# Performance work log

Measured on AMD Instinct MI355X. Metric: run time of the kernel, lower is better.

## Reference

```python
import jax, jax.numpy as jnp
import numpy as np

N = 20000
E = 320000
NEG_SLOPE = 0.2
LN_EPS = 1e-5


def gat_conv(x, W, a_src, a_dst, b, src, dst, heads, ch, concat):
    # x: [N, F_in]; W: [F_in, H*C]; a_src/a_dst: [H, C]; b: [H*C] or [C]
    xl = (x @ W).reshape(N, heads, ch)                      # [N,H,C]
    alpha_src = jnp.sum(xl * a_src, axis=-1)                # [N,H]
    alpha_dst = jnp.sum(xl * a_dst, axis=-1)                # [N,H]
    e = alpha_src[src] + alpha_dst[dst]                     # [E',H]
    e = jax.nn.leaky_relu(e, NEG_SLOPE)
    # segment softmax over incoming edges of each dst node
    m = jax.ops.segment_max(e, dst, num_segments=N)         # [N,H]
    m = jnp.where(jnp.isfinite(m), m, 0.0)
    ex = jnp.exp(e - m[dst])
    denom = jax.ops.segment_sum(ex, dst, num_segments=N)    # [N,H]
    alpha = ex / (denom[dst] + 1e-16)                       # [E',H]
    msg = alpha[:, :, None] * xl[src]                       # [E',H,C]
    out = jax.ops.segment_sum(msg, dst, num_segments=N)     # [N,H,C]
    if concat:
        return out.reshape(N, heads * ch) + b
    return out.mean(axis=1) + b


def layer_norm(x, g, b):
    mu = jnp.mean(x, axis=-1, keepdims=True)
    var = jnp.mean(jnp.square(x - mu), axis=-1, keepdims=True)
    return (x - mu) * jax.lax.rsqrt(var + LN_EPS) * g + b


def setup_inputs() -> dict:
    key = jax.random.key(0)
    ks = jax.random.split(key, 24)
    d = {}
    d["x"] = jax.random.normal(ks[0], (N, 50), dtype=jnp.float32)
    d["edge_index"] = jax.random.randint(ks[1], (2, E), 0, N, dtype=jnp.int64)

    def glorot(k, shape):
        fan = shape[0] + shape[-1]
        return jax.random.normal(k, shape, dtype=jnp.float32) * np.sqrt(2.0 / fan)

    # conv1: 50 -> 256, heads=4, concat
    d["W1"] = glorot(ks[2], (50, 4 * 256))
    d["a_src1"] = glorot(ks[3], (4, 256))
    d["a_dst1"] = glorot(ks[4], (4, 256))
    d["b1"] = jnp.zeros((4 * 256,), jnp.float32)
    # conv2: 1024 -> 256, heads=4, concat
    d["W2"] = glorot(ks[5], (1024, 4 * 256))
    d["a_src2"] = glorot(ks[6], (4, 256))
    d["a_dst2"] = glorot(ks[7], (4, 256))
    d["b2"] = jnp.zeros((4 * 256,), jnp.float32)
    # conv3: 1024 -> 121, heads=6, concat=False
    d["W3"] = glorot(ks[8], (1024, 6 * 121))
    d["a_src3"] = glorot(ks[9], (6, 121))
    d["a_dst3"] = glorot(ks[10], (6, 121))
    d["b3"] = jnp.zeros((121,), jnp.float32)
    # skips
    d["skipW1"] = glorot(ks[11], (50, 1024))
    d["skipb1"] = jnp.zeros((1024,), jnp.float32)
    d["skipW2"] = glorot(ks[12], (1024, 1024))
    d["skipb2"] = jnp.zeros((1024,), jnp.float32)
    # layer norms
    d["g1"] = jnp.ones((1024,), jnp.float32)
    d["beta1"] = jnp.zeros((1024,), jnp.float32)
    d["g2"] = jnp.ones((1024,), jnp.float32)
    d["beta2"] = jnp.zeros((1024,), jnp.float32)
    return d


def reference(x, edge_index, W1, a_src1, a_dst1, b1, W2, a_src2, a_dst2, b2,
              W3, a_src3, a_dst3, b3, skipW1, skipb1, skipW2, skipb2,
              g1, beta1, g2, beta2):
    # add self loops (PyG GATConv default)
    loop = jnp.arange(N, dtype=edge_index.dtype)
    src = jnp.concatenate([edge_index[0], loop])
    dst = jnp.concatenate([edge_index[1], loop])

    h = gat_conv(x, W1, a_src1, a_dst1, b1, src, dst, 4, 256, True)
    h = jax.nn.elu(layer_norm(h + (x @ skipW1 + skipb1), g1, beta1))
    h2 = gat_conv(h, W2, a_src2, a_dst2, b2, src, dst, 4, 256, True)
    h2 = jax.nn.elu(layer_norm(h2 + (h @ skipW2 + skipb2), g2, beta2))
    out = gat_conv(h2, W3, a_src3, a_dst3, b3, src, dst, 6, 121, False)
    return out
```

## Files before the change

### kernel.cpp

```cpp
#include <hip/hip_runtime.h>
#include <hip/hip_bf16.h>
#include <math.h>

typedef __attribute__((ext_vector_type(8))) __bf16 bf16x8;
typedef __attribute__((ext_vector_type(4))) float f32x4;
typedef __attribute__((ext_vector_type(4))) int i32x4;

#if __has_builtin(__builtin_amdgcn_global_load_lds)
#define HAVE_GLD 1
#define GLD16(g, l)                                                                      \
    __builtin_amdgcn_global_load_lds(                                                    \
        (const __attribute__((address_space(1))) unsigned int*)(g),                      \
        (__attribute__((address_space(3))) unsigned int*)(l), 16, 0, 0)
#else
#define HAVE_GLD 0
#endif

__global__ __launch_bounds__(256) void gemm_bt(const __bf16* __restrict__ A,
                                               const __bf16* __restrict__ Bt,
                                               __bf16* __restrict__ C,
                                               int M, int N, int K) {
    __shared__ __bf16 As[128 * 32];
    __shared__ __bf16 Bs[128 * 32];
    const int t = threadIdx.x;
    const int lane = t & 63;
    const int wid = t >> 6;
    const int wm = (wid >> 1) << 6;
    const int wn = (wid & 1) << 6;
    const int bm = blockIdx.x * 128;
    const int bn = blockIdx.y * 128;

    const int srow = (wid << 4) + (lane >> 2);
    const int scol = (lane & 3) << 3;

    f32x4 acc[4][4];
#pragma unroll
    for (int i = 0; i < 4; i++)
#pragma unroll
        for (int j = 0; j < 4; j++) acc[i][j] = (f32x4){0.f, 0.f, 0.f, 0.f};

    const int m16 = lane & 15;
    const int k8 = (lane >> 4) << 3;

    for (int k0 = 0; k0 < K; k0 += 32) {
        __syncthreads();
#if HAVE_GLD
        GLD16(A + (size_t)(bm + srow) * K + k0 + scol, As + srow * 32 + scol);
        GLD16(A + (size_t)(bm + 64 + srow) * K + k0 + scol, As + (64 + srow) * 32 + scol);
        GLD16(Bt + (size_t)(bn + srow) * K + k0 + scol, Bs + srow * 32 + scol);
        GLD16(Bt + (size_t)(bn + 64 + srow) * K + k0 + scol, Bs + (64 + srow) * 32 + scol);
#else
        {
            bf16x8 a0 = *(const bf16x8*)(A + (size_t)(bm + srow) * K + k0 + scol);
            bf16x8 a1 = *(const bf16x8*)(A + (size_t)(bm + 64 + srow) * K + k0 + scol);
            bf16x8 b0 = *(const bf16x8*)(Bt + (size_t)(bn + srow) * K + k0 + scol);
            bf16x8 b1 = *(const bf16x8*)(Bt + (size_t)(bn + 64 + srow) * K + k0 + scol);
            *(bf16x8*)(As + srow * 32 + scol) = a0;
            *(bf16x8*)(As + (64 + srow) * 32 + scol) = a1;
            *(bf16x8*)(Bs + srow * 32 + scol) = b0;
            *(bf16x8*)(Bs + (64 + srow) * 32 + scol) = b1;
        }
#endif
        __syncthreads();
        bf16x8 af[4], bfr[4];
#pragma unroll
        for (int i = 0; i < 4; i++) {
            af[i] = *(const bf16x8*)(As + (wm + 16 * i + m16) * 32 + k8);
            bfr[i] = *(const bf16x8*)(Bs + (wn + 16 * i + m16) * 32 + k8);
        }
#pragma unroll
        for (int i = 0; i < 4; i++)
#pragma unroll
            for (int j = 0; j < 4; j++)
                acc[i][j] = __builtin_amdgcn_mfma_f32_16x16x32_bf16(af[i], bfr[j], acc[i][j], 0, 0, 0);
    }
    const int r4 = (lane >> 4) << 2;
#pragma unroll
    for (int i = 0; i < 4; i++) {
#pragma unroll
        for (int j = 0; j < 4; j++) {
            int col = bn + wn + 16 * j + m16;
#pragma unroll
            for (int r = 0; r < 4; r++) {
                int row = bm + wm + 16 * i + r4 + r;
                C[(size_t)row * N + col] = (__bf16)acc[i][j][r];
            }
        }
    }
}

__global__ void pack_x_k(const float* __restrict__ x, __bf16* __restrict__ xp, int rows_real) {
    int i = blockIdx.x * 256 + threadIdx.x;
    int n = i >> 6, c = i & 63;
    float v = 0.f;
    if (n < rows_real && c < 50) v = x[n * 50 + c];
    xp[(size_t)n * 64 + c] = (__bf16)v;
}

__global__ void transpose_pad_k(const float* __restrict__ W, __bf16* __restrict__ WT,
                                int K, int N, int Kp, int Np) {
    __shared__ float tile[32][33];
    int bx = blockIdx.x, by = blockIdx.y;
    int tx = threadIdx.x & 31, ty = threadIdx.x >> 5;
#pragma unroll
    for (int r = ty; r < 32; r += 8) {
        int k = by * 32 + r, n = bx * 32 + tx;
        float v = 0.f;
        if (k < K && n < N) v = W[(size_t)k * N + n];
        tile[r][tx] = v;
    }
    __syncthreads();
#pragma unroll
    for (int r = ty; r < 32; r += 8) {
        int n = bx * 32 + r, k = by * 32 + tx;
        if (n < Np && k < Kp) WT[(size_t)n * Kp + k] = (__bf16)tile[tx][r];
    }
}

__global__ void transpose_pad_w3_k(const float* __restrict__ W, __bf16* __restrict__ WT) {
    __shared__ float tile[32][33];
    int bx = blockIdx.x, by = blockIdx.y;
    int tx = threadIdx.x & 31, ty = threadIdx.x >> 5;
    int r0 = bx * 32;
    int h = r0 >> 7;
    int c0 = r0 & 127;
#pragma unroll
    for (int r = ty; r < 32; r += 8) {
        int k = by * 32 + r;
        int c = c0 + tx;
        float v = 0.f;
        if (c < 121) v = W[(size_t)k * 726 + h * 121 + c];
        tile[r][tx] = v;
    }
    __syncthreads();
#pragma unroll
    for (int r = ty; r < 32; r += 8) {
        int rr = r0 + r;
        int k = by * 32 + tx;
        WT[(size_t)rr * 1024 + k] = (__bf16)tile[tx][r];
    }
}

__global__ void probe_ei_k(const int* __restrict__ ei, int* __restrict__ flag) {
    if (blockIdx.x == 0 && threadIdx.x == 0) {
        int all0 = 1;
        for (int i = 0; i < 64; i++)
            if (ei[2 * i + 1] != 0) { all0 = 0; break; }
        *flag = all0;
    }
}

__device__ __forceinline__ int load_ei(const int* ei, int idx, int is64) {
    return is64 ? ei[2 * idx] : ei[idx];
}

__global__ void hist_k(const int* __restrict__ ei, const int* __restrict__ flag,
                       int* __restrict__ cnt, int E, int Nn) {
    int e = blockIdx.x * 256 + threadIdx.x;
    if (e >= E + Nn) return;
    int is64 = *flag;
    int d = (e < E) ? load_ei(ei, E + e, is64) : (e - E);
    d = min(max(d, 0), Nn - 1);
    atomicAdd(&cnt[d], 1);
}

__global__ __launch_bounds__(1024) void scan_k(const int* __restrict__ cnt, int* __restrict__ row_ptr,
                                               int Nn) {
    __shared__ int part[1024];
    int t = threadIdx.x;
    int chunk = (Nn + 1023) >> 10;
    int lo = t * chunk;
    int hi = lo + chunk; if (hi > Nn) hi = Nn; if (lo > Nn) lo = Nn;
    int s = 0;
    for (int i = lo; i < hi; i++) s += (cnt[i] + 15) & ~15;
    part[t] = s;
    __syncthreads();
    for (int off = 1; off < 1024; off <<= 1) {
        int v = (t >= off) ? part[t - off] : 0;
        __syncthreads();
        part[t] += v;
        __syncthreads();
    }
    int run = part[t] - s;
    for (int i = lo; i < hi; i++) { row_ptr[i] = run; run += (cnt[i] + 15) & ~15; }
    if (t == 1023) row_ptr[Nn] = part[1023];
}

__global__ void fill_csr_k(const int* __restrict__ ei, const int* __restrict__ flag,
                           const int* __restrict__ row_ptr, int* __restrict__ cursor,
                           int* __restrict__ src_csr, int E, int Nn) {
    int e = blockIdx.x * 256 + threadIdx.x;
    if (e >= E + Nn) return;
    int is64 = *flag;
    int d = (e < E) ? load_ei(ei, E + e, is64) : (e - E);
    int s = (e < E) ? load_ei(ei, e, is64) : (e - E);
    d = min(max(d, 0), Nn - 1);
    s = min(max(s, 0), Nn - 1);
    int slot = row_ptr[d] + atomicAdd(&cursor[d], 1);
    src_csr[slot] = s;
}

__global__ void alpha_k(const __bf16* __restrict__ XL, int ld, const float* __restrict__ a_src,
                        const float* __restrict__ a_dst, float* __restrict__ asrc,
                        float* __restrict__ adst, int Nn, int H, int C, int Cpad) {
    int gw = (blockIdx.x * 256 + threadIdx.x) >> 6;
    int lane = threadIdx.x & 63;
    if (gw >= Nn * H) return;
    int n = gw / H, h = gw - n * H;
    const __bf16* row = XL + (size_t)n * ld + h * Cpad;
    const float* as = a_src + h * C;
    const float* ad = a_dst + h * C;
    float s = 0.f, d = 0.f;
    for (int c = lane; c < C; c += 64) {
        float v = (float)row[c];
        s += v * as[c];
        d += v * ad[c];
    }
#pragma unroll
    for (int off = 32; off; off >>= 1) {
        s += __shfl_down(s, off);
        d += __shfl_down(d, off);
    }
    if (lane == 0) { asrc[n * H + h] = s; adst[n * H + h] = d; }
}

__global__ void attn_k(const int* __restrict__ row_ptr, const int* __restrict__ deg,
                       const int* __restrict__ src_csr,
                       const float* __restrict__ asrc, const float* __restrict__ adst,
                       float* __restrict__ wt, int Nn, int H, int Epad) {
    int gw = (blockIdx.x * 256 + threadIdx.x) >> 6;
    int lane = threadIdx.x & 63;
    if (gw >= Nn) return;
    int n = gw;
    int base = row_ptr[n], dg = deg[n];
    for (int h = 0; h < H; h++) {
        float ad = adst[n * H + h];
        float m = -1e30f;
        for (int s = lane; s < dg; s += 64) {
            float e = asrc[src_csr[base + s] * H + h] + ad;
            e = e > 0.f ? e : 0.2f * e;
            m = fmaxf(m, e);
        }
#pragma unroll
        for (int off = 1; off < 64; off <<= 1) m = fmaxf(m, __shfl_xor(m, off));
        float sum = 0.f;
        for (int s = lane; s < dg; s += 64) {
            float e = asrc[src_csr[base + s] * H + h] + ad;
            e = e > 0.f ? e : 0.2f * e;
            sum += __expf(e - m);
        }
#pragma unroll
        for (int off = 1; off < 64; off <<= 1) sum += __shfl_xor(sum, off);
        float inv = 1.f / (sum + 1e-16f);
        float* wrow = wt + (size_t)h * Epad;
        for (int s = lane; s < dg; s += 64) {
            float e = asrc[src_csr[base + s] * H + h] + ad;
            e = e > 0.f ? e : 0.2f * e;
            wrow[base + s] = __expf(e - m) * inv;
        }
    }
}

__global__ __launch_bounds__(256) void agg_skip6(const __bf16* __restrict__ XL,
                                                 const float* __restrict__ wt,
                                                 const int* __restrict__ row_ptr,
                                                 const int* __restrict__ src_csr,
                                                 const float* __restrict__ bias,
                                                 const float* __restrict__ sb,
                                                 __bf16* __restrict__ SK, int Nn, int Epad) {
    const int cc = blockIdx.x;
    const int n = blockIdx.y * 4 + (threadIdx.x >> 6);
    const int lane = threadIdx.x & 63;
    if (n >= Nn) return;
    const int g = lane >> 4;
    const int p = lane & 15;
    const int col = cc * 128 + p * 8;
    const float* wrow = wt + (size_t)(cc >> 1) * Epad;
    const __bf16* XLc = XL + col;
    const int base = row_ptr[n], end = row_ptr[n + 1];

    float acc[8];
#pragma unroll
    for (int j = 0; j < 8; j++) acc[j] = 0.f;

    for (int e = base; e < end; e += 16) {
        i32x4 si = *(const i32x4*)(src_csr + e + 4 * g);
        f32x4 wv = *(const f32x4*)(wrow + e + 4 * g);
#pragma unroll
        for (int s = 0; s < 4; s++) {
            bf16x8 xv = *(const bf16x8*)(XLc + (size_t)si[s] * 1024);
#pragma unroll
            for (int j = 0; j < 8; j++) acc[j] += wv[s] * (float)xv[j];
        }
    }
#pragma unroll
    for (int j = 0; j < 8; j++) {
        acc[j] += __shfl_xor(acc[j], 16);
        acc[j] += __shfl_xor(acc[j], 32);
    }
    if (lane < 16) {
        size_t o = (size_t)n * 1024 + col;
        bf16x8 sk = *(const bf16x8*)(SK + o);
        bf16x8 res;
#pragma unroll
        for (int j = 0; j < 8; j++)
            res[j] = (__bf16)(acc[j] + bias[col + j] + sb[col + j] + (float)sk[j]);
        *(bf16x8*)(SK + o) = res;
    }
}

__global__ __launch_bounds__(256) void agg_mean6(const __bf16* __restrict__ XL,
                                                 const float* __restrict__ wt,
                                                 const int* __restrict__ row_ptr,
                                                 const int* __restrict__ src_csr,
                                                 __bf16* __restrict__ part, int Nn, int Epad) {
    const int cc = blockIdx.x;
    const int n = blockIdx.y * 4 + (threadIdx.x >> 6);
    const int lane = threadIdx.x & 63;
    if (n >= Nn) return;
    const int g = lane >> 4;
    const int p = lane & 15;
    const int col = cc * 128 + p * 8;
    const float* wrow = wt + (size_t)cc * Epad;
    const __bf16* XLc = XL + col;
    const int base = row_ptr[n], end = row_ptr[n + 1];

    float acc[8];
#pragma unroll
    for (int j = 0; j < 8; j++) acc[j] = 0.f;

    for (int e = base; e < end; e += 16) {
        i32x4 si = *(const i32x4*)(src_csr + e + 4 * g);
        f32x4 wv = *(const f32x4*)(wrow + e + 4 * g);
#pragma unroll
        for (int s = 0; s < 4; s++) {
            bf16x8 xv = *(const bf16x8*)(XLc + (size_t)si[s] * 768);
#pragma unroll
            for (int j = 0; j < 8; j++) acc[j] += wv[s] * (float)xv[j];
        }
    }
#pragma unroll
    for (int j = 0; j < 8; j++) {
        acc[j] += __shfl_xor(acc[j], 16);
        acc[j] += __shfl_xor(acc[j], 32);
    }
    if (lane < 16) {
        size_t o = (size_t)n * 768 + col;
        bf16x8 res;
#pragma unroll
        for (int j = 0; j < 8; j++) res[j] = (__bf16)acc[j];
        *(bf16x8*)(part + o) = res;
    }
}

__global__ __launch_bounds__(128) void reduce_mean_k(const __bf16* __restrict__ part,
                                                     const float* __restrict__ b3,
                                                     float* __restrict__ out, int Nn) {
    int n = blockIdx.x;
    int t = threadIdx.x;
    if (t >= 121) return;
    const __bf16* row = part + (size_t)n * 768;
    float s = 0.f;
#pragma unroll
    for (int h = 0; h < 6; h++) s += (float)row[h * 128 + t];
    out[(size_t)n * 121 + t] = s * (1.f / 6.f) + b3[t];
}

__global__ __launch_bounds__(256) void ln_elu_k(const __bf16* __restrict__ in,
                                                const float* __restrict__ g,
                                                const float* __restrict__ be,
                                                __bf16* __restrict__ out, int rows_real) {
    const int D = 1024;
    int n = blockIdx.x;
    int t = threadIdx.x;
    size_t ro = (size_t)n * D;
    if (n >= rows_real) {
#pragma unroll
        for (int j = 0; j < 4; j++) out[ro + t + 256 * j] = (__bf16)0.f;
        return;
    }
    float v[4];
    float s = 0.f, q = 0.f;
#pragma unroll
    for (int j = 0; j < 4; j++) {
        int c = t + 256 * j;
        float a = (float)in[ro + c];
        v[j] = a;
        s += a;
        q += a * a;
    }
#pragma unroll
    for (int off = 32; off; off >>= 1) {
        s += __shfl_down(s, off);
        q += __shfl_down(q, off);
    }
    __shared__ float rs[8];
    int wid = t >> 6;
    if ((t & 63) == 0) { rs[wid] = s; rs[wid + 4] = q; }
    __syncthreads();
    s = rs[0] + rs[1] + rs[2] + rs[3];
    q = rs[4] + rs[5] + rs[6] + rs[7];
    float mu = s * (1.f / 1024.f);
    float var = q * (1.f / 1024.f) - mu * mu;
    float inv = rsqrtf(fmaxf(var, 0.f) + 1e-5f);
#pragma unroll
    for (int j = 0; j < 4; j++) {
        int c = t + 256 * j;
        float y = (v[j] - mu) * inv * g[c] + be[c];
        y = y > 0.f ? y : expm1f(y);
        out[ro + c] = (__bf16)y;
    }
}

extern "C" void kernel_launch(void* const* d_in, const int* in_sizes, int n_in,
                              void* d_out, int out_size, void* d_ws, size_t ws_size,
                              hipStream_t stream) {
    const float* x   = (const float*)d_in[0];
    const int*   ei  = (const int*)d_in[1];
    const float* W1  = (const float*)d_in[2];
    const float* as1 = (const float*)d_in[3];
    const float* ad1 = (const float*)d_in[4];
    const float* b1  = (const float*)d_in[5];
    const float* W2  = (const float*)d_in[6];
    const float* as2 = (const float*)d_in[7];
    const float* ad2 = (const float*)d_in[8];
    const float* b2  = (const float*)d_in[9];
    const float* W3  = (const float*)d_in[10];
    const float* as3 = (const float*)d_in[11];
    const float* ad3 = (const float*)d_in[12];
    const float* b3  = (const float*)d_in[13];
    const float* sW1 = (const float*)d_in[14];
    const float* sb1 = (const float*)d_in[15];
    const float* sW2 = (const float*)d_in[16];
    const float* sb2 = (const float*)d_in[17];
    const float* g1  = (const float*)d_in[18];
    const float* be1 = (const float*)d_in[19];
    const float* g2  = (const float*)d_in[20];
    const float* be2 = (const float*)d_in[21];
    float* out = (float*)d_out;

    const int Nn = 20000;
    const int E = in_sizes[1] / 2;
    const int E2 = E + Nn;
    const int Ecap = E2 + 16 * Nn;
    const int Mpad = 20096;

    char* p = (char*)d_ws;
    auto alloc = [&](size_t bytes) {
        char* r = p;
        p += (bytes + 255) & ~(size_t)255;
        return r;
    };
    __bf16* W1pT  = (__bf16*)alloc((size_t)1024 * 64 * 2);
    __bf16* sW1T  = (__bf16*)alloc((size_t)1024 * 64 * 2);
    __bf16* W2T   = (__bf16*)alloc((size_t)1024 * 1024 * 2);
    __bf16* sW2T  = (__bf16*)alloc((size_t)1024 * 1024 * 2);
    __bf16* W3pT  = (__bf16*)alloc((size_t)768 * 1024 * 2);
    __bf16* xp    = (__bf16*)alloc((size_t)Mpad * 64 * 2);
    __bf16* XL    = (__bf16*)alloc((size_t)Mpad * 1024 * 2);
    __bf16* SK    = (__bf16*)alloc((size_t)Mpad * 1024 * 2);
    __bf16* H1    = (__bf16*)alloc((size_t)Mpad * 1024 * 2);
    float*  asrcb = (float*)alloc((size_t)Nn * 6 * 4);
    float*  adstb = (float*)alloc((size_t)Nn * 6 * 4);
    float*  wbuf  = (float*)alloc((size_t)6 * Ecap * 4);
    int*    rowp  = (int*)alloc((size_t)(Nn + 1) * 4);
    int*    cnt   = (int*)alloc((size_t)Nn * 4);
    int*    scsr  = (int*)alloc((size_t)Ecap * 4);
    int*    eiflag= (int*)alloc(256);
    __bf16* part  = SK;
    (void)ws_size; (void)n_in; (void)out_size;

    pack_x_k<<<(Mpad * 64) / 256, 256, 0, stream>>>(x, xp, Nn);
    transpose_pad_k<<<dim3(32, 2), 256, 0, stream>>>(W1, W1pT, 50, 1024, 64, 1024);
    transpose_pad_k<<<dim3(32, 2), 256, 0, stream>>>(sW1, sW1T, 50, 1024, 64, 1024);
    transpose_pad_k<<<dim3(32, 32), 256, 0, stream>>>(W2, W2T, 1024, 1024, 1024, 1024);
    transpose_pad_k<<<dim3(32, 32), 256, 0, stream>>>(sW2, sW2T, 1024, 1024, 1024, 1024);
    transpose_pad_w3_k<<<dim3(24, 32), 256, 0, stream>>>(W3, W3pT);

    probe_ei_k<<<1, 64, 0, stream>>>(ei, eiflag);
    hipMemsetAsync(cnt, 0, (size_t)Nn * 4, stream);
    hist_k<<<(E2 + 255) / 256, 256, 0, stream>>>(ei, eiflag, cnt, E, Nn);
    scan_k<<<1, 1024, 0, stream>>>(cnt, rowp, Nn);
    hipMemsetAsync(cnt, 0, (size_t)Nn * 4, stream);
    hipMemsetAsync(scsr, 0, (size_t)Ecap * 4, stream);
    hipMemsetAsync(wbuf, 0, (size_t)6 * Ecap * 4, stream);
    fill_csr_k<<<(E2 + 255) / 256, 256, 0, stream>>>(ei, eiflag, rowp, cnt, scsr, E, Nn);

    gemm_bt<<<dim3(Mpad / 128, 8), 256, 0, stream>>>(xp, W1pT, XL, Mpad, 1024, 64);
    gemm_bt<<<dim3(Mpad / 128, 8), 256, 0, stream>>>(xp, sW1T, SK, Mpad, 1024, 64);
    alpha_k<<<(Nn * 4 * 64) / 256, 256, 0, stream>>>(XL, 1024, as1, ad1, asrcb, adstb, Nn, 4, 256, 256);
    attn_k<<<(Nn + 3) / 4, 256, 0, stream>>>(rowp, cnt, scsr, asrcb, adstb, wbuf, Nn, 4, Ecap);
    agg_skip6<<<dim3(8, (Nn + 3) / 4), 256, 0, stream>>>(XL, wbuf, rowp, scsr, b1, sb1, SK, Nn, Ecap);
    ln_elu_k<<<Mpad, 256, 0, stream>>>(SK, g1, be1, H1, Nn);

    gemm_bt<<<dim3(Mpad / 128, 8), 256, 0, stream>>>(H1, W2T, XL, Mpad, 1024, 1024);
    gemm_bt<<<dim3(Mpad / 128, 8), 256, 0, stream>>>(H1, sW2T, SK, Mpad, 1024, 1024);
    alpha_k<<<(Nn * 4 * 64) / 256, 256, 0, stream>>>(XL, 1024, as2, ad2, asrcb, adstb, Nn, 4, 256, 256);
    attn_k<<<(Nn + 3) / 4, 256, 0, stream>>>(rowp, cnt, scsr, asrcb, adstb, wbuf, Nn, 4, Ecap);
    agg_skip6<<<dim3(8, (Nn + 3) / 4), 256, 0, stream>>>(XL, wbuf, rowp, scsr, b2, sb2, SK, Nn, Ecap);
    ln_elu_k<<<Mpad, 256, 0, stream>>>(SK, g2, be2, H1, Nn);

    gemm_bt<<<dim3(Mpad / 128, 6), 256, 0, stream>>>(H1, W3pT, XL, Mpad, 768, 1024);
    alpha_k<<<(Nn * 6 * 64) / 256, 256, 0, stream>>>(XL, 768, as3, ad3, asrcb, adstb, Nn, 6, 121, 128);
    attn_k<<<(Nn + 3) / 4, 256, 0, stream>>>(rowp, cnt, scsr, asrcb, adstb, wbuf, Nn, 6, Ecap);
    agg_mean6<<<dim3(6, (Nn + 3) / 4), 256, 0, stream>>>(XL, wbuf, rowp, scsr, part, Nn, Ecap);
    reduce_mean_k<<<Nn, 128, 0, stream>>>(part, b3, out, Nn);
}
```

Baseline: 839.5 us.

## Merge prep kernels, fuse paired GEMMs, shrink CSR padding to 8, add fast attention path

Folds the x packing and all weight transposes into one prep kernel. Each pair of GAT and skip GEMMs now runs as a single launch over a concatenated weight matrix. The counter memset is folded into the probe and scan kernels. CSR row padding drops from 16 to 8, so the aggregation loops process 2 neighbours per group instead of 4, which cuts wasted padded gathers. Attention gets a single-pass register path for nodes with degree up to 64, avoiding reloads of the neighbour scores.

```diff
diff --git a/kernel.cpp b/kernel.cpp
--- a/kernel.cpp
+++ b/kernel.cpp
@@ -4,122 +4,110 @@
 
 typedef __attribute__((ext_vector_type(8))) __bf16 bf16x8;
 typedef __attribute__((ext_vector_type(4))) float f32x4;
-typedef __attribute__((ext_vector_type(4))) int i32x4;
 
 #if __has_builtin(__builtin_amdgcn_global_load_lds)
-#define HAVE_GLD 1
 #define GLD16(g, l)                                                                      \
     __builtin_amdgcn_global_load_lds(                                                    \
         (const __attribute__((address_space(1))) unsigned int*)(g),                      \
         (__attribute__((address_space(3))) unsigned int*)(l), 16, 0, 0)
 #else
-#define HAVE_GLD 0
+#define GLD16(g, l) (*(bf16x8*)(l) = *(const bf16x8*)(g))
 #endif
+
+#define GEMM_BODY(A, Bt, K, STORE)                                                       \
+    __shared__ __bf16 As[128 * 32];                                                      \
+    __shared__ __bf16 Bs[128 * 32];                                                      \
+    const int t = threadIdx.x;                                                           \
+    const int lane = t & 63;                                                             \
+    const int wid = t >> 6;                                                              \
+    const int wm = (wid >> 1) << 6;                                                      \
+    const int wn = (wid & 1) << 6;                                                       \
+    const int bm = blockIdx.x * 128;                                                     \
+    const int bn = blockIdx.y * 128;                                                     \
+    const int srow = (wid << 4) + (lane >> 2);                                           \
+    const int scol = (lane & 3) << 3;                                                    \
+    f32x4 acc[4][4];                                                                     \
+    _Pragma("unroll") for (int i = 0; i < 4; i++)                                        \
+        _Pragma("unroll") for (int j = 0; j < 4; j++)                                    \
+            acc[i][j] = (f32x4){0.f, 0.f, 0.f, 0.f};                                     \
+    const int m16 = lane & 15;                                                           \
+    const int k8 = (lane >> 4) << 3;                                                     \
+    for (int k0 = 0; k0 < K; k0 += 32) {                                                 \
+        __syncthreads();                                                                 \
+        GLD16(A + (size_t)(bm + srow) * K + k0 + scol, As + srow * 32 + scol);           \
+        GLD16(A + (size_t)(bm + 64 + srow) * K + k0 + scol, As + (64 + srow) * 32 + scol);\
+        GLD16(Bt + (size_t)(bn + srow) * K + k0 + scol, Bs + srow * 32 + scol);          \
+        GLD16(Bt + (size_t)(bn + 64 + srow) * K + k0 + scol, Bs + (64 + srow) * 32 + scol);\
+        __syncthreads();                                                                 \
+        bf16x8 af[4], bfr[4];                                                            \
+        _Pragma("unroll") for (int i = 0; i < 4; i++) {                                  \
+            af[i] = *(const bf16x8*)(As + (wm + 16 * i + m16) * 32 + k8);                \
+            bfr[i] = *(const bf16x8*)(Bs + (wn + 16 * i + m16) * 32 + k8);               \
+        }                                                                                \
+        _Pragma("unroll") for (int i = 0; i < 4; i++)                                    \
+            _Pragma("unroll") for (int j = 0; j < 4; j++)                                \
+                acc[i][j] = __builtin_amdgcn_mfma_f32_16x16x32_bf16(af[i], bfr[j],       \
+                                                                    acc[i][j], 0, 0, 0); \
+    }                                                                                    \
+    const int r4 = (lane >> 4) << 2;                                                     \
+    STORE
 
 __global__ __launch_bounds__(256) void gemm_bt(const __bf16* __restrict__ A,
                                                const __bf16* __restrict__ Bt,
                                                __bf16* __restrict__ C,
                                                int M, int N, int K) {
-    __shared__ __bf16 As[128 * 32];
-    __shared__ __bf16 Bs[128 * 32];
-    const int t = threadIdx.x;
-    const int lane = t & 63;
-    const int wid = t >> 6;
-    const int wm = (wid >> 1) << 6;
-    const int wn = (wid & 1) << 6;
-    const int bm = blockIdx.x * 128;
-    const int bn = blockIdx.y * 128;
-
-    const int srow = (wid << 4) + (lane >> 2);
-    const int scol = (lane & 3) << 3;
-
-    f32x4 acc[4][4];
-#pragma unroll
-    for (int i = 0; i < 4; i++)
-#pragma unroll
-        for (int j = 0; j < 4; j++) acc[i][j] = (f32x4){0.f, 0.f, 0.f, 0.f};
-
-    const int m16 = lane & 15;
-    const int k8 = (lane >> 4) << 3;
-
-    for (int k0 = 0; k0 < K; k0 += 32) {
-        __syncthreads();
-#if HAVE_GLD
-        GLD16(A + (size_t)(bm + srow) * K + k0 + scol, As + srow * 32 + scol);
-        GLD16(A + (size_t)(bm + 64 + srow) * K + k0 + scol, As + (64 + srow) * 32 + scol);
-        GLD16(Bt + (size_t)(bn + srow) * K + k0 + scol, Bs + srow * 32 + scol);
-        GLD16(Bt + (size_t)(bn + 64 + srow) * K + k0 + scol, Bs + (64 + srow) * 32 + scol);
-#else
-        {
-            bf16x8 a0 = *(const bf16x8*)(A + (size_t)(bm + srow) * K + k0 + scol);
-            bf16x8 a1 = *(const bf16x8*)(A + (size_t)(bm + 64 + srow) * K + k0 + scol);
-            bf16x8 b0 = *(const bf16x8*)(Bt + (size_t)(bn + srow) * K + k0 + scol);
-            bf16x8 b1 = *(const bf16x8*)(Bt + (size_t)(bn + 64 + srow) * K + k0 + scol);
-            *(bf16x8*)(As + srow * 32 + scol) = a0;
-            *(bf16x8*)(As + (64 + srow) * 32 + scol) = a1;
-            *(bf16x8*)(Bs + srow * 32 + scol) = b0;
-            *(bf16x8*)(Bs + (64 + srow) * 32 + scol) = b1;
-        }
-#endif
-        __syncthreads();
-        bf16x8 af[4], bfr[4];
-#pragma unroll
-        for (int i = 0; i < 4; i++) {
-            af[i] = *(const bf16x8*)(As + (wm + 16 * i + m16) * 32 + k8);
-            bfr[i] = *(const bf16x8*)(Bs + (wn + 16 * i + m16) * 32 + k8);
-        }
-#pragma unroll
-        for (int i = 0; i < 4; i++)
-#pragma unroll
-            for (int j = 0; j < 4; j++)
-                acc[i][j] = __builtin_amdgcn_mfma_f32_16x16x32_bf16(af[i], bfr[j], acc[i][j], 0, 0, 0);
-    }
-    const int r4 = (lane >> 4) << 2;
-#pragma unroll
-    for (int i = 0; i < 4; i++) {
-#pragma unroll
-        for (int j = 0; j < 4; j++) {
-            int col = bn + wn + 16 * j + m16;
-#pragma unroll
-            for (int r = 0; r < 4; r++) {
-                int row = bm + wm + 16 * i + r4 + r;
-                C[(size_t)row * N + col] = (__bf16)acc[i][j][r];
-            }
-        }
-    }
-}
-
-__global__ void pack_x_k(const float* __restrict__ x, __bf16* __restrict__ xp, int rows_real) {
-    int i = blockIdx.x * 256 + threadIdx.x;
-    int n = i >> 6, c = i & 63;
-    float v = 0.f;
-    if (n < rows_real && c < 50) v = x[n * 50 + c];
-    xp[(size_t)n * 64 + c] = (__bf16)v;
-}
-
-__global__ void transpose_pad_k(const float* __restrict__ W, __bf16* __restrict__ WT,
-                                int K, int N, int Kp, int Np) {
-    __shared__ float tile[32][33];
-    int bx = blockIdx.x, by = blockIdx.y;
+    GEMM_BODY(A, Bt, K,
+        _Pragma("unroll") for (int i = 0; i < 4; i++)
+            _Pragma("unroll") for (int j = 0; j < 4; j++) {
+                int col = bn + wn + 16 * j + m16;
+                _Pragma("unroll") for (int r = 0; r < 4; r++) {
+                    int row = bm + wm + 16 * i + r4 + r;
+                    C[(size_t)row * N + col] = (__bf16)acc[i][j][r];
+                }
+            })
+}
+
+__global__ __launch_bounds__(256) void gemm_bt2(const __bf16* __restrict__ A,
+                                                const __bf16* __restrict__ Bt,
+                                                __bf16* __restrict__ C0,
+                                                __bf16* __restrict__ C1,
+                                                int M, int K) {
+    GEMM_BODY(A, Bt, K,
+        __bf16* Cp = (bn < 1024) ? C0 : C1;
+        const int cb = bn & 1023;
+        _Pragma("unroll") for (int i = 0; i < 4; i++)
+            _Pragma("unroll") for (int j = 0; j < 4; j++) {
+                int col = cb + wn + 16 * j + m16;
+                _Pragma("unroll") for (int r = 0; r < 4; r++) {
+                    int row = bm + wm + 16 * i + r4 + r;
+                    Cp[(size_t)row * 1024 + col] = (__bf16)acc[i][j][r];
+                }
+            })
+}
+
+__device__ __forceinline__ void transpose_tile(const float* __restrict__ W,
+                                               __bf16* __restrict__ WT,
+                                               int K, int N, int Kp, int Np,
+                                               int bx, int by, float* sm) {
     int tx = threadIdx.x & 31, ty = threadIdx.x >> 5;
 #pragma unroll
     for (int r = ty; r < 32; r += 8) {
         int k = by * 32 + r, n = bx * 32 + tx;
         float v = 0.f;
         if (k < K && n < N) v = W[(size_t)k * N + n];
-        tile[r][tx] = v;
+        sm[r * 33 + tx] = v;
     }
     __syncthreads();
 #pragma unroll
     for (int r = ty; r < 32; r += 8) {
         int n = bx * 32 + r, k = by * 32 + tx;
-        if (n < Np && k < Kp) WT[(size_t)n * Kp + k] = (__bf16)tile[tx][r];
-    }
-}
-
-__global__ void transpose_pad_w3_k(const float* __restrict__ W, __bf16* __restrict__ WT) {
-    __shared__ float tile[32][33];
-    int bx = blockIdx.x, by = blockIdx.y;
+        if (n < Np && k < Kp) WT[(size_t)n * Kp + k] = (__bf16)sm[tx * 33 + r];
+    }
+}
+
+__device__ __forceinline__ void transpose_w3_tile(const float* __restrict__ W,
+                                                  __bf16* __restrict__ WT,
+                                                  int bx, int by, float* sm) {
     int tx = threadIdx.x & 31, ty = threadIdx.x >> 5;
     int r0 = bx * 32;
     int h = r0 >> 7;
@@ -130,22 +118,56 @@
         int c = c0 + tx;
         float v = 0.f;
         if (c < 121) v = W[(size_t)k * 726 + h * 121 + c];
-        tile[r][tx] = v;
+        sm[r * 33 + tx] = v;
     }
     __syncthreads();
 #pragma unroll
     for (int r = ty; r < 32; r += 8) {
         int rr = r0 + r;
         int k = by * 32 + tx;
-        WT[(size_t)rr * 1024 + k] = (__bf16)tile[tx][r];
-    }
-}
-
-__global__ void probe_ei_k(const int* __restrict__ ei, int* __restrict__ flag) {
+        WT[(size_t)rr * 1024 + k] = (__bf16)sm[tx * 33 + r];
+    }
+}
+
+__global__ __launch_bounds__(256) void prep_k(const float* __restrict__ x,
+                                              const float* __restrict__ W1,
+                                              const float* __restrict__ sW1,
+                                              const float* __restrict__ W2,
+                                              const float* __restrict__ sW2,
+                                              const float* __restrict__ W3,
+                                              __bf16* __restrict__ xp,
+                                              __bf16* __restrict__ WTcat1,
+                                              __bf16* __restrict__ WTcat2,
+                                              __bf16* __restrict__ W3pT, int Nn) {
+    __shared__ float sm[32 * 33];
+    int b = blockIdx.x;
+    if (b < 5024) {
+        int i = b * 256 + threadIdx.x;
+        int n = i >> 6, c = i & 63;
+        float v = 0.f;
+        if (n < Nn && c < 50) v = x[n * 50 + c];
+        xp[(size_t)n * 64 + c] = (__bf16)v;
+    } else if (b < 5088) {
+        int i = b - 5024; transpose_tile(W1, WTcat1, 50, 1024, 64, 1024, i % 32, i / 32, sm);
+    } else if (b < 5152) {
+        int i = b - 5088; transpose_tile(sW1, WTcat1 + 1024 * 64, 50, 1024, 64, 1024, i % 32, i / 32, sm);
+    } else if (b < 6176) {
+        int i = b - 5152; transpose_tile(W2, WTcat2, 1024, 1024, 1024, 1024, i % 32, i / 32, sm);
+    } else if (b < 7200) {
+        int i = b - 6176; transpose_tile(sW2, WTcat2 + (size_t)1024 * 1024, 1024, 1024, 1024, 1024, i % 32, i / 32, sm);
+    } else {
+        int i = b - 7200; transpose_w3_tile(W3, W3pT, i % 24, i / 24, sm);
+    }
+}
+
+__global__ void zero_probe_k(const int* __restrict__ ei, int* __restrict__ cnt,
+                             int* __restrict__ flag, int Nn) {
+    int i = blockIdx.x * 256 + threadIdx.x;
+    if (i < Nn) cnt[i] = 0;
     if (blockIdx.x == 0 && threadIdx.x == 0) {
         int all0 = 1;
-        for (int i = 0; i < 64; i++)
-            if (ei[2 * i + 1] != 0) { all0 = 0; break; }
+        for (int k = 0; k < 64; k++)
+            if (ei[2 * k + 1] != 0) { all0 = 0; break; }
         *flag = all0;
     }
 }
@@ -164,7 +186,7 @@
     atomicAdd(&cnt[d], 1);
 }
 
-__global__ __launch_bounds__(1024) void scan_k(const int* __restrict__ cnt, int* __restrict__ row_ptr,
+__global__ __launch_bounds__(1024) void scan_k(int* __restrict__ cnt, int* __restrict__ row_ptr,
                                                int Nn) {
     __shared__ int part[1024];
     int t = threadIdx.x;
@@ -172,7 +194,7 @@
     int lo = t * chunk;
     int hi = lo + chunk; if (hi > Nn) hi = Nn; if (lo > Nn) lo = Nn;
     int s = 0;
-    for (int i = lo; i < hi; i++) s += (cnt[i] + 15) & ~15;
+    for (int i = lo; i < hi; i++) s += (cnt[i] + 7) & ~7;
     part[t] = s;
     __syncthreads();
     for (int off = 1; off < 1024; off <<= 1) {
@@ -182,8 +204,10 @@
         __syncthreads();
     }
     int run = part[t] - s;
-    for (int i = lo; i < hi; i++) { row_ptr[i] = run; run += (cnt[i] + 15) & ~15; }
+    for (int i = lo; i < hi; i++) { row_ptr[i] = run; run += (cnt[i] + 7) & ~7; }
     if (t == 1023) row_ptr[Nn] = part[1023];
+    __syncthreads();
+    for (int i = lo; i < hi; i++) cnt[i] = 0;
 }
 
 __global__ void fill_csr_k(const int* __restrict__ ei, const int* __restrict__ flag,
@@ -227,12 +251,33 @@
 __global__ void attn_k(const int* __restrict__ row_ptr, const int* __restrict__ deg,
                        const int* __restrict__ src_csr,
                        const float* __restrict__ asrc, const float* __restrict__ adst,
-                       float* __restrict__ wt, int Nn, int H, int Epad) {
+                       float* __restrict__ wt, int Nn, int H, int Ecap) {
     int gw = (blockIdx.x * 256 + threadIdx.x) >> 6;
     int lane = threadIdx.x & 63;
     if (gw >= Nn) return;
     int n = gw;
     int base = row_ptr[n], dg = deg[n];
+    if (dg <= 64) {
+        bool v = lane < dg;
+        int src = v ? src_csr[base + lane] : 0;
+        for (int h = 0; h < H; h++) {
+            float ad = adst[n * H + h];
+            float e = -1e30f;
+            if (v) {
+                e = asrc[src * H + h] + ad;
+                e = e > 0.f ? e : 0.2f * e;
+            }
+            float m = e;
+#pragma unroll
+            for (int off = 1; off < 64; off <<= 1) m = fmaxf(m, __shfl_xor(m, off));
+            float ex = v ? __expf(e - m) : 0.f;
+            float sum = ex;
+#pragma unroll
+            for (int off = 1; off < 64; off <<= 1) sum += __shfl_xor(sum, off);
+            if (v) wt[(size_t)h * Ecap + base + lane] = ex / (sum + 1e-16f);
+        }
+        return;
+    }
     for (int h = 0; h < H; h++) {
         float ad = adst[n * H + h];
         float m = -1e30f;
@@ -252,7 +297,7 @@
 #pragma unroll
         for (int off = 1; off < 64; off <<= 1) sum += __shfl_xor(sum, off);
         float inv = 1.f / (sum + 1e-16f);
-        float* wrow = wt + (size_t)h * Epad;
+        float* wrow = wt + (size_t)h * Ecap;
         for (int s = lane; s < dg; s += 64) {
             float e = asrc[src_csr[base + s] * H + h] + ad;
             e = e > 0.f ? e : 0.2f * e;
@@ -261,13 +306,13 @@
     }
 }
 
-__global__ __launch_bounds__(256) void agg_skip6(const __bf16* __restrict__ XL,
+__global__ __launch_bounds__(256) void agg_skip8(const __bf16* __restrict__ XL,
                                                  const float* __restrict__ wt,
                                                  const int* __restrict__ row_ptr,
                                                  const int* __restrict__ src_csr,
                                                  const float* __restrict__ bias,
                                                  const float* __restrict__ sb,
-                                                 __bf16* __restrict__ SK, int Nn, int Epad) {
+                                                 __bf16* __restrict__ SK, int Nn, int Ecap) {
     const int cc = blockIdx.x;
     const int n = blockIdx.y * 4 + (threadIdx.x >> 6);
     const int lane = threadIdx.x & 63;
@@ -275,7 +320,7 @@
     const int g = lane >> 4;
     const int p = lane & 15;
     const int col = cc * 128 + p * 8;
-    const float* wrow = wt + (size_t)(cc >> 1) * Epad;
+    const float* wrow = wt + (size_t)(cc >> 1) * Ecap;
     const __bf16* XLc = XL + col;
     const int base = row_ptr[n], end = row_ptr[n + 1];
 
@@ -283,15 +328,13 @@
 #pragma unroll
     for (int j = 0; j < 8; j++) acc[j] = 0.f;
 
-    for (int e = base; e < end; e += 16) {
-        i32x4 si = *(const i32x4*)(src_csr + e + 4 * g);
-        f32x4 wv = *(const f32x4*)(wrow + e + 4 * g);
-#pragma unroll
-        for (int s = 0; s < 4; s++) {
-            bf16x8 xv = *(const bf16x8*)(XLc + (size_t)si[s] * 1024);
-#pragma unroll
-            for (int j = 0; j < 8; j++) acc[j] += wv[s] * (float)xv[j];
-        }
+    for (int e = base; e < end; e += 8) {
+        int2 si = *(const int2*)(src_csr + e + 2 * g);
+        float2 wv = *(const float2*)(wrow + e + 2 * g);
+        bf16x8 xa = *(const bf16x8*)(XLc + (size_t)si.x * 1024);
+        bf16x8 xb = *(const bf16x8*)(XLc + (size_t)si.y * 1024);
+#pragma unroll
+        for (int j = 0; j < 8; j++) acc[j] += wv.x * (float)xa[j] + wv.y * (float)xb[j];
     }
 #pragma unroll
     for (int j = 0; j < 8; j++) {
@@ -309,11 +352,11 @@
     }
 }
 
-__global__ __launch_bounds__(256) void agg_mean6(const __bf16* __restrict__ XL,
+__global__ __launch_bounds__(256) void agg_mean8(const __bf16* __restrict__ XL,
                                                  const float* __restrict__ wt,
                                                  const int* __restrict__ row_ptr,
                                                  const int* __restrict__ src_csr,
-                                                 __bf16* __restrict__ part, int Nn, int Epad) {
+                                                 __bf16* __restrict__ part, int Nn, int Ecap) {
     const int cc = blockIdx.x;
     const int n = blockIdx.y * 4 + (threadIdx.x >> 6);
     const int lane = threadIdx.x & 63;
@@ -321,7 +364,7 @@
     const int g = lane >> 4;
     const int p = lane & 15;
     const int col = cc * 128 + p * 8;
-    const float* wrow = wt + (size_t)cc * Epad;
+    const float* wrow = wt + (size_t)cc * Ecap;
     const __bf16* XLc = XL + col;
     const int base = row_ptr[n], end = row_ptr[n + 1];
 
@@ -329,15 +372,13 @@
 #pragma unroll
     for (int j = 0; j < 8; j++) acc[j] = 0.f;
 
-    for (int e = base; e < end; e += 16) {
-        i32x4 si = *(const i32x4*)(src_csr + e + 4 * g);
-        f32x4 wv = *(const f32x4*)(wrow + e + 4 * g);
-#pragma unroll
-        for (int s = 0; s < 4; s++) {
-            bf16x8 xv = *(const bf16x8*)(XLc + (size_t)si[s] * 768);
-#pragma unroll
-            for (int j = 0; j < 8; j++) acc[j] += wv[s] * (float)xv[j];
-        }
+    for (int e = base; e < end; e += 8) {
+        int2 si = *(const int2*)(src_csr + e + 2 * g);
+        float2 wv = *(const float2*)(wrow + e + 2 * g);
+        bf16x8 xa = *(const bf16x8*)(XLc + (size_t)si.x * 768);
+        bf16x8 xb = *(const bf16x8*)(XLc + (size_t)si.y * 768);
+#pragma unroll
+        for (int j = 0; j < 8; j++) acc[j] += wv.x * (float)xa[j] + wv.y * (float)xb[j];
     }
 #pragma unroll
     for (int j = 0; j < 8; j++) {
@@ -442,7 +483,7 @@
     const int Nn = 20000;
     const int E = in_sizes[1] / 2;
     const int E2 = E + Nn;
-    const int Ecap = E2 + 16 * Nn;
+    const int Ecap = E2 + 8 * Nn;
     const int Mpad = 20096;
 
     char* p = (char*)d_ws;
@@ -451,58 +492,47 @@
         p += (bytes + 255) & ~(size_t)255;
         return r;
     };
-    __bf16* W1pT  = (__bf16*)alloc((size_t)1024 * 64 * 2);
-    __bf16* sW1T  = (__bf16*)alloc((size_t)1024 * 64 * 2);
-    __bf16* W2T   = (__bf16*)alloc((size_t)1024 * 1024 * 2);
-    __bf16* sW2T  = (__bf16*)alloc((size_t)1024 * 1024 * 2);
-    __bf16* W3pT  = (__bf16*)alloc((size_t)768 * 1024 * 2);
-    __bf16* xp    = (__bf16*)alloc((size_t)Mpad * 64 * 2);
-    __bf16* XL    = (__bf16*)alloc((size_t)Mpad * 1024 * 2);
-    __bf16* SK    = (__bf16*)alloc((size_t)Mpad * 1024 * 2);
-    __bf16* H1    = (__bf16*)alloc((size_t)Mpad * 1024 * 2);
-    float*  asrcb = (float*)alloc((size_t)Nn * 6 * 4);
-    float*  adstb = (float*)alloc((size_t)Nn * 6 * 4);
-    float*  wbuf  = (float*)alloc((size_t)6 * Ecap * 4);
-    int*    rowp  = (int*)alloc((size_t)(Nn + 1) * 4);
-    int*    cnt   = (int*)alloc((size_t)Nn * 4);
-    int*    scsr  = (int*)alloc((size_t)Ecap * 4);
-    int*    eiflag= (int*)alloc(256);
-    __bf16* part  = SK;
+    __bf16* WTcat1 = (__bf16*)alloc((size_t)2048 * 64 * 2);
+    __bf16* WTcat2 = (__bf16*)alloc((size_t)2048 * 1024 * 2);
+    __bf16* W3pT   = (__bf16*)alloc((size_t)768 * 1024 * 2);
+    __bf16* xp     = (__bf16*)alloc((size_t)Mpad * 64 * 2);
+    __bf16* XL     = (__bf16*)alloc((size_t)Mpad * 1024 * 2);
+    __bf16* SK     = (__bf16*)alloc((size_t)Mpad * 1024 * 2);
+    __bf16* H1     = (__bf16*)alloc((size_t)Mpad * 1024 * 2);
+    float*  asrcb  = (float*)alloc((size_t)Nn * 6 * 4);
+    float*  adstb  = (float*)alloc((size_t)Nn * 6 * 4);
+    float*  wbuf   = (float*)alloc((size_t)6 * Ecap * 4);
+    int*    rowp   = (int*)alloc((size_t)(Nn + 1) * 4);
+    int*    cnt    = (int*)alloc((size_t)Nn * 4);
+    int*    scsr   = (int*)alloc((size_t)Ecap * 4);
+    int*    eiflag = (int*)alloc(256);
+    __bf16* part   = SK;
     (void)ws_size; (void)n_in; (void)out_size;
 
-    pack_x_k<<<(Mpad * 64) / 256, 256, 0, stream>>>(x, xp, Nn);
-    transpose_pad_k<<<dim3(32, 2), 256, 0, stream>>>(W1, W1pT, 50, 1024, 64, 1024);
-    transpose_pad_k<<<dim3(32, 2), 256, 0, stream>>>(sW1, sW1T, 50, 1024, 64, 1024);
-    transpose_pad_k<<<dim3(32, 32), 256, 0, stream>>>(W2, W2T, 1024, 1024, 1024, 1024);
-    transpose_pad_k<<<dim3(32, 32), 256, 0, stream>>>(sW2, sW2T, 1024, 1024, 1024, 1024);
-    transpose_pad_w3_k<<<dim3(24, 32), 256, 0, stream>>>(W3, W3pT);
-
-    probe_ei_k<<<1, 64, 0, stream>>>(ei, eiflag);
-    hipMemsetAsync(cnt, 0, (size_t)Nn * 4, stream);
+    prep_k<<<7968, 256, 0, stream>>>(x, W1, sW1, W2, sW2, W3, xp, WTcat1, WTcat2, W3pT, Nn);
+
+    zero_probe_k<<<(Nn + 255) / 256, 256, 0, stream>>>(ei, cnt, eiflag, Nn);
     hist_k<<<(E2 + 255) / 256, 256, 0, stream>>>(ei, eiflag, cnt, E, Nn);
     scan_k<<<1, 1024, 0, stream>>>(cnt, rowp, Nn);
-    hipMemsetAsync(cnt, 0, (size_t)Nn * 4, stream);
-    hipMemsetAsync(scsr, 0, (size_t)Ecap * 4, stream);
-    hipMemsetAsync(wbuf, 0, (size_t)6 * Ecap * 4, stream);
+    (void)hipMemsetAsync(scsr, 0, (size_t)Ecap * 4, stream);
+    (void)hipMemsetAsync(wbuf, 0, (size_t)6 * Ecap * 4, stream);
     fill_csr_k<<<(E2 + 255) / 256, 256, 0, stream>>>(ei, eiflag, rowp, cnt, scsr, E, Nn);
 
-    gemm_bt<<<dim3(Mpad / 128, 8), 256, 0, stream>>>(xp, W1pT, XL, Mpad, 1024, 64);
-    gemm_bt<<<dim3(Mpad / 128, 8), 256, 0, stream>>>(xp, sW1T, SK, Mpad, 1024, 64);
+    gemm_bt2<<<dim3(Mpad / 128, 16), 256, 0, stream>>>(xp, WTcat1, XL, SK, Mpad, 64);
     alpha_k<<<(Nn * 4 * 64) / 256, 256, 0, stream>>>(XL, 1024, as1, ad1, asrcb, adstb, Nn, 4, 256, 256);
     attn_k<<<(Nn + 3) / 4, 256, 0, stream>>>(rowp, cnt, scsr, asrcb, adstb, wbuf, Nn, 4, Ecap);
-    agg_skip6<<<dim3(8, (Nn + 3) / 4), 256, 0, stream>>>(XL, wbuf, rowp, scsr, b1, sb1, SK, Nn, Ecap);
+    agg_skip8<<<dim3(8, (Nn + 3) / 4), 256, 0, stream>>>(XL, wbuf, rowp, scsr, b1, sb1, SK, Nn, Ecap);
     ln_elu_k<<<Mpad, 256, 0, stream>>>(SK, g1, be1, H1, Nn);
 
-    gemm_bt<<<dim3(Mpad / 128, 8), 256, 0, stream>>>(H1, W2T, XL, Mpad, 1024, 1024);
-    gemm_bt<<<dim3(Mpad / 128, 8), 256, 0, stream>>>(H1, sW2T, SK, Mpad, 1024, 1024);
+    gemm_bt2<<<dim3(Mpad / 128, 16), 256, 0, stream>>>(H1, WTcat2, XL, SK, Mpad, 1024);
     alpha_k<<<(Nn * 4 * 64) / 256, 256, 0, stream>>>(XL, 1024, as2, ad2, asrcb, adstb, Nn, 4, 256, 256);
     attn_k<<<(Nn + 3) / 4, 256, 0, stream>>>(rowp, cnt, scsr, asrcb, adstb, wbuf, Nn, 4, Ecap);
-    agg_skip6<<<dim3(8, (Nn + 3) / 4), 256, 0, stream>>>(XL, wbuf, rowp, scsr, b2, sb2, SK, Nn, Ecap);
+    agg_skip8<<<dim3(8, (Nn + 3) / 4), 256, 0, stream>>>(XL, wbuf, rowp, scsr, b2, sb2, SK, Nn, Ecap);
     ln_elu_k<<<Mpad, 256, 0, stream>>>(SK, g2, be2, H1, Nn);
 
     gemm_bt<<<dim3(Mpad / 128, 6), 256, 0, stream>>>(H1, W3pT, XL, Mpad, 768, 1024);
     alpha_k<<<(Nn * 6 * 64) / 256, 256, 0, stream>>>(XL, 768, as3, ad3, asrcb, adstb, Nn, 6, 121, 128);
     attn_k<<<(Nn + 3) / 4, 256, 0, stream>>>(rowp, cnt, scsr, asrcb, adstb, wbuf, Nn, 6, Ecap);
-    agg_mean6<<<dim3(6, (Nn + 3) / 4), 256, 0, stream>>>(XL, wbuf, rowp, scsr, part, Nn, Ecap);
+    agg_mean8<<<dim3(6, (Nn + 3) / 4), 256, 0, stream>>>(XL, wbuf, rowp, scsr, part, Nn, Ecap);
     reduce_mean_k<<<Nn, 128, 0, stream>>>(part, b3, out, Nn);
 }
```

New measurement: 797.5 us. -5.0%, faster.
